# Performance work log

Measured on AMD Instinct MI355X. Metric: run time of the kernel, lower is better.

Reference implementation:

```python
import jax, jax.numpy as jnp
import numpy as np

B, C, S = 4, 2, 4096          # batch, in_channels, samples
K, NK, OUT = 64, 32, 512      # kernel_size, num_kernels, out_channels


def setup_inputs() -> dict:
    key = jax.random.key(0)
    k1, k2, k3, k4 = jax.random.split(key, 4)
    x = jax.random.normal(k1, (B, C, S), dtype=jnp.float32)
    # LearnableSTFTFunction.learnable_weights: (num_kernels, kernel_size), torch.randn init
    stft_w = jax.random.normal(k2, (NK, K), dtype=jnp.float32)
    # Conv1d(in=C*K*NK, out=OUT, kernel=1): weight (OUT, C*K*NK), bias (OUT,)
    conv_w = jax.random.normal(k3, (OUT, C * K * NK), dtype=jnp.float32) * 0.02
    conv_b = jax.random.normal(k4, (OUT,), dtype=jnp.float32) * 0.02
    return {"x": x, "stft_w": stft_w, "conv_w": conv_w, "conv_b": conv_b}


def reference(x, stft_w, conv_w, conv_b):
    b, c, s = x.shape
    nk, k = stft_w.shape
    # F.pad(x, (0, K-1)) then unfold(-1, K, 1) -> (b, c, s, K) sliding windows
    xp = jnp.pad(x, ((0, 0), (0, 0), (0, k - 1)))
    idx = jnp.arange(s)[:, None] + jnp.arange(k)[None, :]  # (s, K)
    win = xp[:, :, idx]  # (b, c, s, K)
    # einsum('ijklm,lm->ijkml') with l=1 broadcast: elementwise per-kernel weighting,
    # no reduction over m -> (b, c, s, K, NK)
    xw = jnp.einsum('bcsm,lm->bcsml', win, stft_w)
    # torch raw reshape (row-major), deliberately mixing s into channel blocks
    xr = xw.reshape(b, c * k * nk, s)
    # 1x1 Conv1d == channel matmul, then ReLU
    out = jnp.einsum('bis,oi->bos', xr, conv_w) + conv_b[None, :, None]
    return jax.nn.relu(out)
```

## Files before the change

### kernel.cpp

```cpp
#include <hip/hip_runtime.h>
#include <hip/hip_bf16.h>

#define NB   4
#define NC   2
#define NS   4096
#define NOUT 512
#define UPAD 80
#define MT   128

typedef short  short8_t  __attribute__((ext_vector_type(8)));
typedef float  float16_t __attribute__((ext_vector_type(16)));

__device__ __forceinline__ short bf16s(float f) {
    union { __hip_bfloat16 b; short s; } u;
    u.b = __float2bfloat16(f);
    return u.s;
}
__device__ __forceinline__ float s2f(unsigned short s) {
    union { unsigned int u; float f; } v;
    v.u = ((unsigned int)s) << 16;
    return v.f;
}

template<int KCN>
__global__ __launch_bounds__(256)
void gemm_partials(const float* __restrict__ x,
                   const float* __restrict__ conv_w,
                   unsigned short* __restrict__ hpart)
{
    constexpr int KC  = 4096 / KCN;
    constexpr int XSZ = KC + 56;
    __shared__ __align__(16) short xS[16][XSZ];

    const int blk = blockIdx.x;
    const int kc  = blk % KCN;
    const int ot  = (blk / KCN) & 3;
    const int b   = blk / (KCN * 4);

    const int K0 = kc * KC;
    const int c  = K0 >> 11;
    const int tb = K0 & 2047;

    const int tid = threadIdx.x;
    const float* xc = x + (size_t)(b * NC + c) * NS;

    for (int i = tid; i < XSZ; i += 256) {
        int ge = (tb + i) * 2;
        float fe = (ge     < NS) ? xc[ge]     : 0.0f;
        float fo = (ge + 1 < NS) ? xc[ge + 1] : 0.0f;
        short se = bf16s(fe), so = bf16s(fo);
        #pragma unroll
        for (int r = 0; r < 8; ++r) {
            int j = i - r;
            if (j >= 0) { xS[r][j] = se; xS[8 + r][j] = so; }
        }
    }
    __syncthreads();

    const int wave = tid >> 6;
    const int lane = tid & 63;
    const int l31  = lane & 31;
    const int q    = lane >> 5;
    const int kq   = q * 8;

    const float* wrow = conv_w + (size_t)(ot * MT + wave * 32 + l31) * 4096 + K0;

    float16_t acc[3];
    #pragma unroll
    for (int nt = 0; nt < 3; ++nt)
        #pragma unroll
        for (int e = 0; e < 16; ++e) acc[nt][e] = 0.0f;

    int arr[3], hb[3];
    #pragma unroll
    for (int nt = 0; nt < 3; ++nt) {
        int uu = nt * 32 + l31;
        int h  = uu >> 1;
        arr[nt] = (uu & 1) * 8 + (h & 7);
        hb[nt]  = h & ~7;
    }

    #pragma unroll
    for (int step = 0; step < KC / 16; ++step) {
        const int kl = step * 16 + kq;
        float4 a0 = *(const float4*)(wrow + kl);
        float4 a1 = *(const float4*)(wrow + kl + 4);
        short8_t af = { bf16s(a0.x), bf16s(a0.y), bf16s(a0.z), bf16s(a0.w),
                        bf16s(a1.x), bf16s(a1.y), bf16s(a1.z), bf16s(a1.w) };
        #pragma unroll
        for (int nt = 0; nt < 3; ++nt) {
            short8_t bf = *(const short8_t*)&xS[arr[nt]][kl + hb[nt]];
            acc[nt] = __builtin_amdgcn_mfma_f32_32x32x16_bf16(af, bf, acc[nt], 0, 0, 0);
        }
    }

    unsigned short* hp = hpart + (size_t)(kc * NB + b) * NOUT * UPAD;
    #pragma unroll
    for (int nt = 0; nt < 3; ++nt) {
        int uu = nt * 32 + l31;
        if (uu < UPAD) {
            #pragma unroll
            for (int reg = 0; reg < 16; ++reg) {
                int row = (reg & 3) + 8 * (reg >> 2) + 4 * q;
                int o   = ot * MT + wave * 32 + row;
                hp[(size_t)o * UPAD + uu] = (unsigned short)bf16s(acc[nt][reg]);
            }
        }
    }
}

template<int KCN>
__global__ __launch_bounds__(256)
void reduce_epilogue(const unsigned short* __restrict__ hpart,
                     const float* __restrict__ stft_w,
                     const float* __restrict__ conv_b,
                     float* __restrict__ out)
{
    __shared__ float Hs[65];
    const int tid = threadIdx.x;
    const int bid = blockIdx.x;
    const int b = bid >> 9;
    const int o = bid & 511;

    if (tid < 65) {
        const unsigned short* hp0 = hpart + ((size_t)b * NOUT + o) * UPAD + tid;
        float h = 0.0f;
        #pragma unroll
        for (int s = 0; s < KCN; ++s)
            h += s2f(hp0[(size_t)s * NB * NOUT * UPAD]);
        Hs[tid] = h;
    }
    __syncthreads();

    const float bias = conv_b[o];
    float* ob = out + (size_t)(b * NOUT + o) * NS;
    #pragma unroll
    for (int it = 0; it < 4; ++it) {
        int s4 = (it * 256 + tid) * 4;
        int r  = s4 >> 11;
        int qq = s4 & 2047;
        int m  = qq >> 5;
        int l  = qq & 31;
        float h = Hs[r + m];
        float v0 = fmaf(stft_w[(l + 0) * 64 + m], h, bias);
        float v1 = fmaf(stft_w[(l + 1) * 64 + m], h, bias);
        float v2 = fmaf(stft_w[(l + 2) * 64 + m], h, bias);
        float v3 = fmaf(stft_w[(l + 3) * 64 + m], h, bias);
        float4 res;
        res.x = v0 > 0.0f ? v0 : 0.0f;
        res.y = v1 > 0.0f ? v1 : 0.0f;
        res.z = v2 > 0.0f ? v2 : 0.0f;
        res.w = v3 > 0.0f ? v3 : 0.0f;
        *(float4*)(ob + s4) = res;
    }
}

template<int KCN>
static void launch_pair(const float* x, const float* stft_w, const float* conv_w,
                        const float* conv_b, float* out, unsigned short* ws,
                        hipStream_t stream)
{
    gemm_partials<KCN><<<dim3(NB * 4 * KCN), dim3(256), 0, stream>>>(x, conv_w, ws);
    reduce_epilogue<KCN><<<dim3(NB * NOUT), dim3(256), 0, stream>>>(ws, stft_w, conv_b, out);
}

extern "C" void kernel_launch(void* const* d_in, const int* in_sizes, int n_in,
                              void* d_out, int out_size, void* d_ws, size_t ws_size,
                              hipStream_t stream) {
    const float* x      = (const float*)d_in[0];
    const float* stft_w = (const float*)d_in[1];
    const float* conv_w = (const float*)d_in[2];
    const float* conv_b = (const float*)d_in[3];
    float* out = (float*)d_out;
    unsigned short* ws = (unsigned short*)d_ws;

    const size_t per_slice = (size_t)NB * NOUT * UPAD * sizeof(unsigned short);
    if      (ws_size >= 32 * per_slice) launch_pair<32>(x, stft_w, conv_w, conv_b, out, ws, stream);
    else if (ws_size >= 16 * per_slice) launch_pair<16>(x, stft_w, conv_w, conv_b, out, ws, stream);
    else if (ws_size >=  8 * per_slice) launch_pair<8 >(x, stft_w, conv_w, conv_b, out, ws, stream);
    else                                launch_pair<4 >(x, stft_w, conv_w, conv_b, out, ws, stream);
}
```

Measured before the change: 90.68 us.

## Stage weight tile in LDS, split reduction across thread halves, add fused fallback

The GEMM-partials kernel now converts its 128-row conv_w tile to bf16 once into LDS, then feeds the MFMA A operand from LDS instead of reloading and converting global floats inside the K loop. The reduce kernel splits the sum over K-chunk slices between two thread groups to shorten the serial load chain. A new fused FP32 kernel with no workspace replaces the KCN=4 path when the workspace is small. The large LDS allocation lowers occupancy, and the fused path only runs for small workspaces.

Result: faster. 88.28 us (-2.6%).

```diff
diff --git a/kernel.cpp b/kernel.cpp
--- a/kernel.cpp
+++ b/kernel.cpp
@@ -6,9 +6,9 @@
 #define NS   4096
 #define NOUT 512
 #define UPAD 80
-#define MT   128
 
 typedef short  short8_t  __attribute__((ext_vector_type(8)));
+typedef short  short4_t  __attribute__((ext_vector_type(4)));
 typedef float  float16_t __attribute__((ext_vector_type(16)));
 
 __device__ __forceinline__ short bf16s(float f) {
@@ -28,8 +28,12 @@
                    const float* __restrict__ conv_w,
                    unsigned short* __restrict__ hpart)
 {
-    constexpr int KC  = 4096 / KCN;
-    constexpr int XSZ = KC + 56;
+    constexpr int KC      = 4096 / KCN;
+    constexpr int XSZ     = KC + 56;
+    constexpr int ASTRIDE = KC + 8;
+    static_assert(KCN >= 8, "A-tile LDS exceeds 160KB below KCN=8");
+
+    __shared__ __align__(16) short aS[128 * ASTRIDE];
     __shared__ __align__(16) short xS[16][XSZ];
 
     const int blk = blockIdx.x;
@@ -40,10 +44,9 @@
     const int K0 = kc * KC;
     const int c  = K0 >> 11;
     const int tb = K0 & 2047;
-
     const int tid = threadIdx.x;
+
     const float* xc = x + (size_t)(b * NC + c) * NS;
-
     for (int i = tid; i < XSZ; i += 256) {
         int ge = (tb + i) * 2;
         float fe = (ge     < NS) ? xc[ge]     : 0.0f;
@@ -55,15 +58,30 @@
             if (j >= 0) { xS[r][j] = se; xS[8 + r][j] = so; }
         }
     }
+
+    {
+        const int rr = tid >> 5;
+        const int cc = (tid & 31) * 4;
+        const float* wbase = conv_w + (size_t)(ot * 128) * 4096 + K0;
+        #pragma unroll
+        for (int cb = 0; cb < KC; cb += 128) {
+            #pragma unroll
+            for (int it = 0; it < 16; ++it) {
+                int row = it * 8 + rr;
+                float4 v = *(const float4*)(wbase + (size_t)row * 4096 + cb + cc);
+                short4_t p = { bf16s(v.x), bf16s(v.y), bf16s(v.z), bf16s(v.w) };
+                *(short4_t*)&aS[row * ASTRIDE + cb + cc] = p;
+            }
+        }
+    }
     __syncthreads();
 
     const int wave = tid >> 6;
     const int lane = tid & 63;
     const int l31  = lane & 31;
     const int q    = lane >> 5;
-    const int kq   = q * 8;
-
-    const float* wrow = conv_w + (size_t)(ot * MT + wave * 32 + l31) * 4096 + K0;
+
+    const short* arow = &aS[(wave * 32 + l31) * ASTRIDE];
 
     float16_t acc[3];
     #pragma unroll
@@ -82,11 +100,8 @@
 
     #pragma unroll
     for (int step = 0; step < KC / 16; ++step) {
-        const int kl = step * 16 + kq;
-        float4 a0 = *(const float4*)(wrow + kl);
-        float4 a1 = *(const float4*)(wrow + kl + 4);
-        short8_t af = { bf16s(a0.x), bf16s(a0.y), bf16s(a0.z), bf16s(a0.w),
-                        bf16s(a1.x), bf16s(a1.y), bf16s(a1.z), bf16s(a1.w) };
+        const int kl = step * 16 + q * 8;
+        short8_t af = *(const short8_t*)(arow + kl);
         #pragma unroll
         for (int nt = 0; nt < 3; ++nt) {
             short8_t bf = *(const short8_t*)&xS[arr[nt]][kl + hb[nt]];
@@ -102,7 +117,7 @@
             #pragma unroll
             for (int reg = 0; reg < 16; ++reg) {
                 int row = (reg & 3) + 8 * (reg >> 2) + 4 * q;
-                int o   = ot * MT + wave * 32 + row;
+                int o   = ot * 128 + wave * 32 + row;
                 hp[(size_t)o * UPAD + uu] = (unsigned short)bf16s(acc[nt][reg]);
             }
         }
@@ -116,19 +131,28 @@
                      const float* __restrict__ conv_b,
                      float* __restrict__ out)
 {
-    __shared__ float Hs[65];
+    __shared__ float HsA[65], HsB[65];
     const int tid = threadIdx.x;
     const int bid = blockIdx.x;
     const int b = bid >> 9;
     const int o = bid & 511;
 
+    constexpr int HALF = KCN / 2;
+    const size_t slice = (size_t)NB * NOUT * UPAD;
+
     if (tid < 65) {
         const unsigned short* hp0 = hpart + ((size_t)b * NOUT + o) * UPAD + tid;
         float h = 0.0f;
         #pragma unroll
-        for (int s = 0; s < KCN; ++s)
-            h += s2f(hp0[(size_t)s * NB * NOUT * UPAD]);
-        Hs[tid] = h;
+        for (int s = 0; s < HALF; ++s) h += s2f(hp0[(size_t)s * slice]);
+        HsA[tid] = h;
+    } else if (tid >= 128 && tid < 193) {
+        const unsigned short* hp0 = hpart + ((size_t)b * NOUT + o) * UPAD + (tid - 128)
+                                  + (size_t)HALF * slice;
+        float h = 0.0f;
+        #pragma unroll
+        for (int s = 0; s < KCN - HALF; ++s) h += s2f(hp0[(size_t)s * slice]);
+        HsB[tid - 128] = h;
     }
     __syncthreads();
 
@@ -141,6 +165,112 @@
         int qq = s4 & 2047;
         int m  = qq >> 5;
         int l  = qq & 31;
+        float h = HsA[r + m] + HsB[r + m];
+        float v0 = fmaf(stft_w[(l + 0) * 64 + m], h, bias);
+        float v1 = fmaf(stft_w[(l + 1) * 64 + m], h, bias);
+        float v2 = fmaf(stft_w[(l + 2) * 64 + m], h, bias);
+        float v3 = fmaf(stft_w[(l + 3) * 64 + m], h, bias);
+        float4 res;
+        res.x = v0 > 0.0f ? v0 : 0.0f;
+        res.y = v1 > 0.0f ? v1 : 0.0f;
+        res.z = v2 > 0.0f ? v2 : 0.0f;
+        res.w = v3 > 0.0f ? v3 : 0.0f;
+        *(float4*)(ob + s4) = res;
+    }
+}
+
+__device__ __forceinline__ int swz(int i) { return i + (i >> 5); }
+
+__global__ __launch_bounds__(256, 3)
+void fused_cnn(const float* __restrict__ x,
+               const float* __restrict__ stft_w,
+               const float* __restrict__ conv_w,
+               const float* __restrict__ conv_b,
+               float* __restrict__ out)
+{
+    __shared__ float xs[2 * 4290];
+    __shared__ float ws_[4224];
+    __shared__ float Hs[65];
+
+    const int tid = threadIdx.x;
+    const int bid = blockIdx.x;
+    const int b = bid >> 9;
+    const int o = bid & 511;
+
+    for (int c = 0; c < NC; ++c) {
+        const float* xb = x + (size_t)(b * NC + c) * NS;
+        float* dst = xs + c * 4290;
+        #pragma unroll
+        for (int it = 0; it < 4; ++it) {
+            int i0 = (it * 256 + tid) * 4;
+            float4 v = *(const float4*)(xb + i0);
+            dst[swz(i0 + 0)] = v.x; dst[swz(i0 + 1)] = v.y;
+            dst[swz(i0 + 2)] = v.z; dst[swz(i0 + 3)] = v.w;
+        }
+        if (tid < 64) dst[swz(4096 + tid)] = 0.0f;
+    }
+    {
+        const float* wrow = conv_w + (size_t)o * 4096;
+        #pragma unroll
+        for (int it = 0; it < 4; ++it) {
+            int i0 = (it * 256 + tid) * 4;
+            float4 v = *(const float4*)(wrow + i0);
+            ws_[swz(i0 + 0)] = v.x; ws_[swz(i0 + 1)] = v.y;
+            ws_[swz(i0 + 2)] = v.z; ws_[swz(i0 + 3)] = v.w;
+        }
+    }
+    __syncthreads();
+
+    const int wave = tid >> 6;
+    const int lane = tid & 63;
+    const int u0 = wave << 4;
+
+    float acc[17];
+    #pragma unroll
+    for (int i = 0; i < 17; ++i) acc[i] = 0.0f;
+
+    for (int g = 0; g < 8; ++g) {
+        int G = lane + (g << 6);
+        int c = G >> 8;
+        int t0 = (G & 255) << 3;
+        int wb = c * 2048 + t0;
+        float w[8];
+        #pragma unroll
+        for (int j = 0; j < 8; ++j) w[j] = ws_[swz(wb + j)];
+        const float* xcs = xs + c * 4290;
+        int xb0 = 2 * t0 + u0;
+        #pragma unroll
+        for (int d = 0; d <= 30; ++d) {
+            float xv = xcs[swz(xb0 + d)];
+            #pragma unroll
+            for (int j = 0; j < 8; ++j) {
+                int uu = d - 2 * j;
+                if (uu >= 0 && uu < 17) acc[uu] += w[j] * xv;
+            }
+        }
+    }
+    #pragma unroll
+    for (int uu = 0; uu < 17; ++uu) {
+        float v = acc[uu];
+        #pragma unroll
+        for (int off = 1; off < 64; off <<= 1) v += __shfl_xor(v, off, 64);
+        acc[uu] = v;
+    }
+    if (lane == 0)
+        #pragma unroll
+        for (int uu = 0; uu < 17; ++uu)
+            if (uu < 16 || wave == 3) Hs[u0 + uu] = acc[uu];
+    __syncthreads();
+
+    const float bias = conv_b[o];
+    float* ob = out + (size_t)(b * NOUT + o) * NS;
+    #pragma unroll
+    for (int it = 0; it < 4; ++it) {
+        int s4 = (it * 256 + tid) * 4;
+        int r = s4 >> 11;
+        int qq = s4 & 2047;
+        int m = qq >> 5;
+        int l = qq & 31;
         float h = Hs[r + m];
         float v0 = fmaf(stft_w[(l + 0) * 64 + m], h, bias);
         float v1 = fmaf(stft_w[(l + 1) * 64 + m], h, bias);
@@ -178,5 +308,6 @@
     if      (ws_size >= 32 * per_slice) launch_pair<32>(x, stft_w, conv_w, conv_b, out, ws, stream);
     else if (ws_size >= 16 * per_slice) launch_pair<16>(x, stft_w, conv_w, conv_b, out, ws, stream);
     else if (ws_size >=  8 * per_slice) launch_pair<8 >(x, stft_w, conv_w, conv_b, out, ws, stream);
-    else                                launch_pair<4 >(x, stft_w, conv_w, conv_b, out, ws, stream);
-}
+    else
+        fused_cnn<<<dim3(NB * NOUT), dim3(256), 0, stream>>>(x, stft_w, conv_w, conv_b, out);
+}
```
